# Kernel optimization log

Measured on AMD Instinct MI355X. Metric: run time of the kernel, lower is better.

## Reference

```python
import jax, jax.numpy as jnp
import numpy as np

HIDDEN = 1024
B, LQ, LK = 8, 2048, 2048


def setup_inputs() -> dict:
    key = jax.random.key(0)
    k1, k2, k3 = jax.random.split(key, 3)
    query = jax.random.normal(k1, (B, LQ, HIDDEN), dtype=jnp.float32)
    key_t = jax.random.normal(k2, (B, LK, HIDDEN), dtype=jnp.float32)
    # multiplicative binary mask on scores (float 0/1)
    attention_mask = jax.random.randint(k3, (B, LQ, LK), 0, 2).astype(jnp.float32)
    return {"query": query, "key": key_t, "attention_mask": attention_mask}


def reference(query, key, attention_mask):
    sqrt_dim = np.sqrt(HIDDEN).astype(np.float32)
    # [B, Lq, Lk] scores, scaled then multiplicatively masked (NOT additive)
    score = jnp.einsum("bqd,bkd->bqk", query, key) / sqrt_dim
    score = score * attention_mask
    attn = jax.nn.softmax(score, axis=-1)
    # NOTE: original module multiplies attn by KEY (not value)
    context = jnp.einsum("bqk,bkd->bqd", attn, key)
    return (context, attn)
```

## Files before the change

kernel.cpp:

```cpp
#include <hip/hip_runtime.h>
#include <hip/hip_bf16.h>


typedef __attribute__((ext_vector_type(8))) short bf16x8;
typedef __attribute__((ext_vector_type(4))) float f32x4;
typedef __attribute__((ext_vector_type(4))) unsigned u32x4;
typedef __attribute__((ext_vector_type(2))) unsigned u32x2;

constexpr int BATCH = 8;
constexpr int LQ    = 2048;
constexpr int LKK   = 2048;
constexpr int DH    = 1024;
constexpr float SCALE = 0.03125f;

#define GAS(p) ((const __attribute__((address_space(1))) void*)(p))
#define LAS(p) ((__attribute__((address_space(3))) void*)(p))

__device__ __forceinline__ unsigned lds_addr(const unsigned short* p) {
    return (unsigned)(unsigned long long)
        (const __attribute__((address_space(3))) unsigned short*)p;
}

__device__ __forceinline__ bf16x8 dsr_b128(unsigned off) {
    bf16x8 r;
    asm volatile("ds_read_b128 %0, %1" : "=v"(r) : "v"(off));
    return r;
}

__device__ __forceinline__ unsigned pack_bf16x2(float x0, float x1) {
    unsigned a = __builtin_bit_cast(unsigned, x0) + 0x8000u;
    unsigned b = __builtin_bit_cast(unsigned, x1) + 0x8000u;
    return __builtin_amdgcn_perm(b, a, 0x07060302u);
}

__global__ __launch_bounds__(256)
void cvt_kernel(const float* __restrict__ Q, const float* __restrict__ K,
                unsigned short* __restrict__ Qb, unsigned short* __restrict__ Kb) {
    const int bid = blockIdx.x;
    const float* src; unsigned short* dst; size_t off;
    if (bid < 4096) { src = Q; dst = Qb; off = (size_t)bid * 4096; }
    else            { src = K; dst = Kb; off = (size_t)(bid - 4096) * 4096; }
    off += (size_t)threadIdx.x * 16;
    const f32x4 a = *(const f32x4*)(src + off);
    const f32x4 b = *(const f32x4*)(src + off + 4);
    const f32x4 c = *(const f32x4*)(src + off + 8);
    const f32x4 d = *(const f32x4*)(src + off + 12);
    u32x4 v0, v1;
    v0[0] = pack_bf16x2(a[0], a[1]); v0[1] = pack_bf16x2(a[2], a[3]);
    v0[2] = pack_bf16x2(b[0], b[1]); v0[3] = pack_bf16x2(b[2], b[3]);
    v1[0] = pack_bf16x2(c[0], c[1]); v1[1] = pack_bf16x2(c[2], c[3]);
    v1[2] = pack_bf16x2(d[0], d[1]); v1[3] = pack_bf16x2(d[2], d[3]);
    *(u32x4*)(dst + off)     = v0;
    *(u32x4*)(dst + off + 8) = v1;
}

__global__ __launch_bounds__(256)
void kt_kernel(const float* __restrict__ K, unsigned short* __restrict__ KT) {
    __shared__ unsigned short T[64 * 68];
    const int b  = blockIdx.z;
    const int k0 = blockIdx.y * 64;
    const int d0 = blockIdx.x * 64;
    const int t  = threadIdx.x;
    const int k4 = (t >> 4) * 4;
    const int d4 = (t & 15) * 4;
    f32x4 rk[4];
    const float* Kp = K + ((size_t)b * LKK + k0 + k4) * DH + d0 + d4;
#pragma unroll
    for (int j = 0; j < 4; ++j) rk[j] = *(const f32x4*)(Kp + (size_t)j * DH);
#pragma unroll
    for (int c = 0; c < 4; ++c) {
        u32x2 w;
        w[0] = pack_bf16x2(rk[0][c], rk[1][c]);
        w[1] = pack_bf16x2(rk[2][c], rk[3][c]);
        *(u32x2*)&T[(d4 + c) * 68 + k4] = w;
    }
    __syncthreads();
    const int d  = t >> 2;
    const int kc = (t & 3) * 16;
    u32x2 a0 = *(const u32x2*)&T[d * 68 + kc];
    u32x2 a1 = *(const u32x2*)&T[d * 68 + kc + 4];
    u32x2 a2 = *(const u32x2*)&T[d * 68 + kc + 8];
    u32x2 a3 = *(const u32x2*)&T[d * 68 + kc + 12];
    unsigned short* dst = KT + ((size_t)b * DH + d0 + d) * LKK + k0 + kc;
    u32x4 w0; w0[0] = a0[0]; w0[1] = a0[1]; w0[2] = a1[0]; w0[3] = a1[1];
    u32x4 w1; w1[0] = a2[0]; w1[1] = a2[1]; w1[2] = a3[0]; w1[3] = a3[1];
    *(u32x4*)dst       = w0;
    *(u32x4*)(dst + 8) = w1;
}

template<int LDA, int LDB, int NT>
__device__ __forceinline__ void gemm8_mainloop(
    const unsigned short* __restrict__ Ab,
    const unsigned short* __restrict__ Bb,
    unsigned short* lA, unsigned short* lB,
    f32x4 (&acc)[8][4])
{
    const int tid  = threadIdx.x;
    const int lane = tid & 63;
    const int wid  = tid >> 6;
    const int wm   = (wid & 1) * 128;
    const int wn   = (wid >> 1) * 64;
    const int lrow = lane & 15;
    const int quad = lane >> 4;
    const int slotsw = (quad ^ ((lrow >> 1) & 3)) * 8;

    const int srow0 = wid * 32 + (lane >> 2);
    const int srow1 = srow0 + 16;
    const int sc    = ((lane & 3) ^ ((lane >> 3) & 3)) * 8;

    auto stage = [&](int I) {
        if (I >= 4 * NT) return;
        const int tile = I >> 2;
        const int h    = I & 3;
        const int kh   = h >> 1;
        const int kb   = tile * 64 + kh * 32 + sc;
        const unsigned short* s = (h & 1) ? Bb : Ab;
        const int ld            = (h & 1) ? LDB : LDA;
        unsigned short* d = ((h & 1) ? lB : lA)
                          + (tile & 1) * 16384 + kh * 8192 + wid * 1024;
        __builtin_amdgcn_global_load_lds(GAS(s + (size_t)srow0 * ld + kb), LAS(d),       16, 0, 0);
        __builtin_amdgcn_global_load_lds(GAS(s + (size_t)srow1 * ld + kb), LAS(d + 512), 16, 0, 0);
    };

#pragma unroll
    for (int i = 0; i < 8; ++i)
#pragma unroll
        for (int j = 0; j < 4; ++j) acc[i][j] = (f32x4){0.f, 0.f, 0.f, 0.f};

#pragma unroll
    for (int I = 0; I < 6; ++I) stage(I);
    asm volatile("s_waitcnt vmcnt(8)" ::: "memory");
    __builtin_amdgcn_s_barrier();

    auto tilebody = [&](int T, int par) {
        bf16x8 bfr[4];
#pragma unroll
        for (int q = 0; q < 4; ++q) {
            const int kh = (q >> 1) * 8192;
            const int mh = (q & 1) * 4;
            if ((q & 1) == 0) {
#pragma unroll
                for (int nf = 0; nf < 4; ++nf)
                    bfr[nf] = dsr_b128(lds_addr(&lB[par + kh + (wn + nf * 16 + lrow) * 32 + slotsw]));
            }
            bf16x8 af[4];
#pragma unroll
            for (int mf = 0; mf < 4; ++mf)
                af[mf] = dsr_b128(lds_addr(&lA[par + kh + (wm + (mh + mf) * 16 + lrow) * 32 + slotsw]));

            if (q == 0)      stage(4 * T + 6);
            else if (q == 1) stage(4 * T + 7);
            else if (q == 2) { stage(4 * T + 8); stage(4 * T + 9); }

            __builtin_amdgcn_s_barrier();
            asm volatile("s_waitcnt lgkmcnt(0)" ::: "memory");
            __builtin_amdgcn_sched_barrier(0);
            __builtin_amdgcn_s_setprio(1);
#pragma unroll
            for (int mf = 0; mf < 4; ++mf)
#pragma unroll
                for (int nf = 0; nf < 4; ++nf)
                    acc[mh + mf][nf] = __builtin_amdgcn_mfma_f32_16x16x32_bf16(
                        af[mf], bfr[nf], acc[mh + mf][nf], 0, 0, 0);
            __builtin_amdgcn_s_setprio(0);
            if (q == 1) {
                if (T < NT - 1)      asm volatile("s_waitcnt vmcnt(8)" ::: "memory");
                else                 asm volatile("s_waitcnt vmcnt(0)" ::: "memory");
            } else if (q == 3) {
                if (T < NT - 2)      asm volatile("s_waitcnt vmcnt(8)" ::: "memory");
                else if (T == NT - 2) asm volatile("s_waitcnt vmcnt(4)" ::: "memory");
            }
            __builtin_amdgcn_s_barrier();
        }
    };

    for (int T = 0; T < NT; T += 2) {
        tilebody(T,     0);
        tilebody(T + 1, 16384);
    }
}

__global__ __launch_bounds__(512, 2)
void qk8(const unsigned short* __restrict__ Qb, const unsigned short* __restrict__ Kb,
         const float* __restrict__ M, float* __restrict__ S) {
    __shared__ __align__(16) unsigned short lA[32768];
    __shared__ __align__(16) unsigned short lB[32768];

    const int l   = blockIdx.x;
    const int swz = (l & 7) * 64 + (l >> 3);
    const int b   = swz >> 6;
    const int my  = (swz >> 3) & 7;
    const int nx  = swz & 7;
    const int q0  = my * 256;
    const int n0  = nx * 256;

    const unsigned short* Ap = Qb + ((size_t)b * LQ  + q0) * DH;
    const unsigned short* Bp = Kb + ((size_t)b * LKK + n0) * DH;

    f32x4 acc[8][4];
    gemm8_mainloop<DH, DH, DH / 64>(Ap, Bp, lA, lB, acc);

    const int lane = threadIdx.x & 63;
    const int wid  = threadIdx.x >> 6;
    const int wm   = (wid & 1) * 128;
    const int wn   = (wid >> 1) * 64;
    const int lrow = lane & 15;
    const int quad = lane >> 4;

    const size_t base = (size_t)b * LQ * LKK;
#pragma unroll
    for (int mf = 0; mf < 8; ++mf) {
#pragma unroll
        for (int r = 0; r < 4; ++r) {
            const int row = q0 + wm + mf * 16 + quad * 4 + r;
            const size_t rb = base + (size_t)row * LKK;
#pragma unroll
            for (int nf = 0; nf < 4; ++nf) {
                const int col = n0 + wn + nf * 16 + lrow;
                S[rb + col] = acc[mf][nf][r] * SCALE * M[rb + col];
            }
        }
    }
}

__global__ __launch_bounds__(256)
void softmax_kernel(float* __restrict__ A, unsigned short* __restrict__ ab) {
    const int row  = blockIdx.x * 4 + (threadIdx.x >> 6);
    const int lane = threadIdx.x & 63;
    float* p = A + (size_t)row * LKK;

    f32x4 v[8];
#pragma unroll
    for (int i = 0; i < 8; ++i) v[i] = *(const f32x4*)(p + i * 256 + lane * 4);

    float m = v[0][0];
#pragma unroll
    for (int i = 0; i < 8; ++i)
#pragma unroll
        for (int j = 0; j < 4; ++j) m = fmaxf(m, v[i][j]);
#pragma unroll
    for (int o = 32; o >= 1; o >>= 1) m = fmaxf(m, __shfl_xor(m, o, 64));

    float s = 0.f;
#pragma unroll
    for (int i = 0; i < 8; ++i)
#pragma unroll
        for (int j = 0; j < 4; ++j) { v[i][j] = __expf(v[i][j] - m); s += v[i][j]; }
#pragma unroll
    for (int o = 32; o >= 1; o >>= 1) s += __shfl_xor(s, o, 64);
    const float inv = 1.f / s;

#pragma unroll
    for (int i = 0; i < 8; ++i) {
#pragma unroll
        for (int j = 0; j < 4; ++j) v[i][j] *= inv;
        *(f32x4*)(p + i * 256 + lane * 4) = v[i];
    }

    if (ab) {
        unsigned short* q = ab + (size_t)row * LKK;
#pragma unroll
        for (int i = 0; i < 8; ++i) {
            u32x2 w;
            w[0] = pack_bf16x2(v[i][0], v[i][1]);
            w[1] = pack_bf16x2(v[i][2], v[i][3]);
            *(u32x2*)(q + i * 256 + lane * 4) = w;
        }
    }
}

__global__ __launch_bounds__(512, 2)
void pk8(const unsigned short* __restrict__ Pb, const unsigned short* __restrict__ KT,
         float* __restrict__ C) {
    __shared__ __align__(16) unsigned short lA[32768];
    __shared__ __align__(16) unsigned short lB[32768];

    const int l   = blockIdx.x;
    const int swz = (l & 7) * 32 + (l >> 3);
    const int b   = swz >> 5;
    const int my  = (swz >> 2) & 7;
    const int nx  = swz & 3;
    const int q0  = my * 256;
    const int n0  = nx * 256;

    const unsigned short* Ap = Pb + ((size_t)b * LQ + q0) * LKK;
    const unsigned short* Bp = KT + ((size_t)b * DH + n0) * LKK;

    f32x4 acc[8][4];
    gemm8_mainloop<LKK, LKK, LKK / 64>(Ap, Bp, lA, lB, acc);

    const int lane = threadIdx.x & 63;
    const int wid  = threadIdx.x >> 6;
    const int wm   = (wid & 1) * 128;
    const int wn   = (wid >> 1) * 64;
    const int lrow = lane & 15;
    const int quad = lane >> 4;

    const size_t cb = (size_t)b * LQ * DH;
#pragma unroll
    for (int mf = 0; mf < 8; ++mf) {
#pragma unroll
        for (int r = 0; r < 4; ++r) {
            const int row = q0 + wm + mf * 16 + quad * 4 + r;
            const size_t rbase = cb + (size_t)row * DH;
#pragma unroll
            for (int nf = 0; nf < 4; ++nf)
                C[rbase + n0 + wn + nf * 16 + lrow] = acc[mf][nf][r];
        }
    }
}

constexpr int BM = 128, BN = 128, TK = 32;
constexpr int LDSS = 40;
__global__ __launch_bounds__(256, 2)
void pk_kernel(const float* __restrict__ P, const float* __restrict__ K,
               float* __restrict__ C) {
    __shared__ unsigned short lA[BM * LDSS];
    __shared__ unsigned short lB[BN * LDSS];

    const int b  = blockIdx.z;
    const int q0 = blockIdx.y * BM;
    const int n0 = blockIdx.x * BN;
    const float* Pp = P + (size_t)b * LQ * LKK + (size_t)q0 * LKK;
    const float* Kb = K + (size_t)b * LKK * DH;

    const int tid  = threadIdx.x;
    const int lane = tid & 63;
    const int wid  = tid >> 6;
    const int wm   = (wid & 1) * 64;
    const int wn   = (wid >> 1) * 64;
    const int lrow = lane & 15;
    const int quad = lane >> 4;

    f32x4 acc[4][4];
#pragma unroll
    for (int i = 0; i < 4; ++i)
#pragma unroll
        for (int j = 0; j < 4; ++j) acc[i][j] = (f32x4){0.f, 0.f, 0.f, 0.f};

    const int srow = tid >> 3;
    const int skq  = (tid & 7) << 2;
    const int tdb  = tid >> 3;
    const int tkb  = tid & 7;

    for (int k0 = 0; k0 < LKK; k0 += TK) {
        __syncthreads();
#pragma unroll
        for (int i = 0; i < 4; ++i) {
            const int row = i * 32 + srow;
            const f32x4 va = *(const f32x4*)(Pp + (size_t)row * LKK + k0 + skq);
            unsigned* pa = (unsigned*)&lA[row * LDSS + skq];
            pa[0] = pack_bf16x2(va[0], va[1]);
            pa[1] = pack_bf16x2(va[2], va[3]);
        }
        f32x4 rk[4];
#pragma unroll
        for (int j = 0; j < 4; ++j)
            rk[j] = *(const f32x4*)(Kb + (size_t)(k0 + tkb * 4 + j) * DH + n0 + tdb * 4);
#pragma unroll
        for (int c = 0; c < 4; ++c) {
            unsigned* pb = (unsigned*)&lB[(tdb * 4 + c) * LDSS + tkb * 4];
            pb[0] = pack_bf16x2(rk[0][c], rk[1][c]);
            pb[1] = pack_bf16x2(rk[2][c], rk[3][c]);
        }
        __syncthreads();

        bf16x8 af[4], bfr[4];
#pragma unroll
        for (int i = 0; i < 4; ++i) {
            af[i]  = *(const bf16x8*)&lA[(wm + i * 16 + lrow) * LDSS + quad * 8];
            bfr[i] = *(const bf16x8*)&lB[(wn + i * 16 + lrow) * LDSS + quad * 8];
        }
#pragma unroll
        for (int i = 0; i < 4; ++i)
#pragma unroll
            for (int j = 0; j < 4; ++j)
                acc[i][j] = __builtin_amdgcn_mfma_f32_16x16x32_bf16(af[i], bfr[j], acc[i][j], 0, 0, 0);
    }

    const size_t cb = (size_t)b * LQ * DH;
#pragma unroll
    for (int i = 0; i < 4; ++i) {
#pragma unroll
        for (int r = 0; r < 4; ++r) {
            const int row = q0 + wm + i * 16 + quad * 4 + r;
            const size_t rbase = cb + (size_t)row * DH;
#pragma unroll
            for (int j = 0; j < 4; ++j)
                C[rbase + n0 + wn + j * 16 + lrow] = acc[i][j][r];
        }
    }
}

extern "C" void kernel_launch(void* const* d_in, const int* in_sizes, int n_in,
                              void* d_out, int out_size, void* d_ws, size_t ws_size,
                              hipStream_t stream) {
    const float* Q = (const float*)d_in[0];
    const float* K = (const float*)d_in[1];
    const float* M = (const float*)d_in[2];

    constexpr size_t QEL  = (size_t)BATCH * LQ * DH;
    constexpr size_t AEL  = (size_t)BATCH * LQ * LKK;
    constexpr size_t KTEL = (size_t)BATCH * DH * LKK;

    float* ctx  = (float*)d_out;
    float* attn = ctx + QEL;

    unsigned short* Qb = (unsigned short*)ctx;
    unsigned short* Kb = Qb + QEL;

    const bool wsOK = ws_size >= (KTEL + AEL) * sizeof(unsigned short);
    unsigned short* KT = (unsigned short*)d_ws;
    unsigned short* ab = KT + KTEL;

    cvt_kernel<<<dim3(8192), 256, 0, stream>>>(Q, K, Qb, Kb);
    if (wsOK)
        kt_kernel<<<dim3(DH / 64, LKK / 64, BATCH), 256, 0, stream>>>(K, KT);
    qk8<<<dim3(BATCH * (LQ / 256) * (LKK / 256)), 512, 0, stream>>>(Qb, Kb, M, attn);
    softmax_kernel<<<dim3(BATCH * LQ / 4), 256, 0, stream>>>(attn, wsOK ? ab : nullptr);
    if (wsOK)
        pk8<<<dim3(BATCH * (LQ / 256) * (DH / 256)), 512, 0, stream>>>(ab, KT, ctx);
    else
        pk_kernel<<<dim3(DH / BN, LQ / BM, BATCH), 256, 0, stream>>>(attn, K, ctx);
}
```

Before: 574.7 us.

## Fuse exp into QK epilogue, defer softmax normalization into PV epilogue

The QK GEMM epilogue now applies scale, mask and exp directly and writes bf16 unnormalized probabilities, replacing the fp32 score buffer and the separate max/exp softmax pass. A lighter sum_norm kernel reads the bf16 values, computes the per-row reciprocal sum, writes the normalized fp32 attention output and stores the reciprocals. The PV GEMM multiplies its output rows by those reciprocals. K's bf16 conversion also moves into the transpose kernel, so K is read once instead of twice. The aim is to cut large fp32 round trips through HBM. The cost is dropping max subtraction, which risks overflow for larger score ranges, and deriving the attention output from bf16-rounded exponentials, which lowers its precision.

```diff
diff --git a/kernel.cpp b/kernel.cpp
--- a/kernel.cpp
+++ b/kernel.cpp
@@ -31,6 +31,10 @@
     unsigned a = __builtin_bit_cast(unsigned, x0) + 0x8000u;
     unsigned b = __builtin_bit_cast(unsigned, x1) + 0x8000u;
     return __builtin_amdgcn_perm(b, a, 0x07060302u);
+}
+
+__device__ __forceinline__ unsigned short pack_bf16(float x) {
+    return (unsigned short)((__builtin_bit_cast(unsigned, x) + 0x8000u) >> 16);
 }
 
 __global__ __launch_bounds__(256)
@@ -55,7 +59,8 @@
 }
 
 __global__ __launch_bounds__(256)
-void kt_kernel(const float* __restrict__ K, unsigned short* __restrict__ KT) {
+void kt_kernel(const float* __restrict__ K, unsigned short* __restrict__ KT,
+               unsigned short* __restrict__ Kb) {
     __shared__ unsigned short T[64 * 68];
     const int b  = blockIdx.z;
     const int k0 = blockIdx.y * 64;
@@ -67,6 +72,14 @@
     const float* Kp = K + ((size_t)b * LKK + k0 + k4) * DH + d0 + d4;
 #pragma unroll
     for (int j = 0; j < 4; ++j) rk[j] = *(const f32x4*)(Kp + (size_t)j * DH);
+    unsigned short* Kbp = Kb + ((size_t)b * LKK + k0 + k4) * DH + d0 + d4;
+#pragma unroll
+    for (int j = 0; j < 4; ++j) {
+        u32x2 w;
+        w[0] = pack_bf16x2(rk[j][0], rk[j][1]);
+        w[1] = pack_bf16x2(rk[j][2], rk[j][3]);
+        *(u32x2*)(Kbp + (size_t)j * DH) = w;
+    }
 #pragma unroll
     for (int c = 0; c < 4; ++c) {
         u32x2 w;
@@ -164,10 +177,10 @@
                         af[mf], bfr[nf], acc[mh + mf][nf], 0, 0, 0);
             __builtin_amdgcn_s_setprio(0);
             if (q == 1) {
-                if (T < NT - 1)      asm volatile("s_waitcnt vmcnt(8)" ::: "memory");
-                else                 asm volatile("s_waitcnt vmcnt(0)" ::: "memory");
+                if (T < NT - 1)       asm volatile("s_waitcnt vmcnt(8)" ::: "memory");
+                else                  asm volatile("s_waitcnt vmcnt(0)" ::: "memory");
             } else if (q == 3) {
-                if (T < NT - 2)      asm volatile("s_waitcnt vmcnt(8)" ::: "memory");
+                if (T < NT - 2)       asm volatile("s_waitcnt vmcnt(8)" ::: "memory");
                 else if (T == NT - 2) asm volatile("s_waitcnt vmcnt(4)" ::: "memory");
             }
             __builtin_amdgcn_s_barrier();
@@ -180,9 +193,11 @@
     }
 }
 
+template<bool FUSED>
 __global__ __launch_bounds__(512, 2)
 void qk8(const unsigned short* __restrict__ Qb, const unsigned short* __restrict__ Kb,
-         const float* __restrict__ M, float* __restrict__ S) {
+         const float* __restrict__ M, float* __restrict__ S,
+         unsigned short* __restrict__ ab) {
     __shared__ __align__(16) unsigned short lA[32768];
     __shared__ __align__(16) unsigned short lB[32768];
 
@@ -217,10 +232,55 @@
 #pragma unroll
             for (int nf = 0; nf < 4; ++nf) {
                 const int col = n0 + wn + nf * 16 + lrow;
-                S[rb + col] = acc[mf][nf][r] * SCALE * M[rb + col];
+                if (FUSED) {
+                    const float e = __expf(acc[mf][nf][r] * SCALE * M[rb + col]);
+                    ab[rb + col] = pack_bf16(e);
+                } else {
+                    S[rb + col] = acc[mf][nf][r] * SCALE * M[rb + col];
+                }
             }
         }
     }
+}
+
+__global__ __launch_bounds__(256)
+void sum_norm(const unsigned short* __restrict__ ab, float* __restrict__ attn,
+              float* __restrict__ inv) {
+    const int row  = blockIdx.x * 4 + (threadIdx.x >> 6);
+    const int lane = threadIdx.x & 63;
+    const unsigned short* q = ab + (size_t)row * LKK;
+
+    u32x4 w[4];
+#pragma unroll
+    for (int i = 0; i < 4; ++i) w[i] = *(const u32x4*)(q + i * 512 + lane * 8);
+
+    float v[32];
+    float s = 0.f;
+#pragma unroll
+    for (int i = 0; i < 4; ++i)
+#pragma unroll
+        for (int j = 0; j < 4; ++j) {
+            const unsigned u = w[i][j];
+            const float lo = __builtin_bit_cast(float, u << 16);
+            const float hi = __builtin_bit_cast(float, u & 0xFFFF0000u);
+            v[i * 8 + j * 2]     = lo;
+            v[i * 8 + j * 2 + 1] = hi;
+            s += lo + hi;
+        }
+#pragma unroll
+    for (int o = 32; o >= 1; o >>= 1) s += __shfl_xor(s, o, 64);
+    const float iv = 1.f / s;
+
+    float* p = attn + (size_t)row * LKK;
+#pragma unroll
+    for (int i = 0; i < 4; ++i) {
+        f32x4 o0, o1;
+#pragma unroll
+        for (int j = 0; j < 4; ++j) { o0[j] = v[i * 8 + j] * iv; o1[j] = v[i * 8 + 4 + j] * iv; }
+        *(f32x4*)(p + i * 512 + lane * 8)     = o0;
+        *(f32x4*)(p + i * 512 + lane * 8 + 4) = o1;
+    }
+    if (lane == 0) inv[row] = iv;
 }
 
 __global__ __launch_bounds__(256)
@@ -271,7 +331,7 @@
 
 __global__ __launch_bounds__(512, 2)
 void pk8(const unsigned short* __restrict__ Pb, const unsigned short* __restrict__ KT,
-         float* __restrict__ C) {
+         const float* __restrict__ Inv, float* __restrict__ C) {
     __shared__ __align__(16) unsigned short lA[32768];
     __shared__ __align__(16) unsigned short lB[32768];
 
@@ -296,16 +356,18 @@
     const int lrow = lane & 15;
     const int quad = lane >> 4;
 
+    const float* Ivp = Inv + (size_t)b * LQ;
     const size_t cb = (size_t)b * LQ * DH;
 #pragma unroll
     for (int mf = 0; mf < 8; ++mf) {
 #pragma unroll
         for (int r = 0; r < 4; ++r) {
             const int row = q0 + wm + mf * 16 + quad * 4 + r;
+            const float iv = Ivp[row];
             const size_t rbase = cb + (size_t)row * DH;
 #pragma unroll
             for (int nf = 0; nf < 4; ++nf)
-                C[rbase + n0 + wn + nf * 16 + lrow] = acc[mf][nf][r];
+                C[rbase + n0 + wn + nf * 16 + lrow] = acc[mf][nf][r] * iv;
         }
     }
 }
@@ -402,6 +464,7 @@
     constexpr size_t QEL  = (size_t)BATCH * LQ * DH;
     constexpr size_t AEL  = (size_t)BATCH * LQ * LKK;
     constexpr size_t KTEL = (size_t)BATCH * DH * LKK;
+    constexpr size_t REL  = (size_t)BATCH * LQ;
 
     float* ctx  = (float*)d_out;
     float* attn = ctx + QEL;
@@ -409,17 +472,24 @@
     unsigned short* Qb = (unsigned short*)ctx;
     unsigned short* Kb = Qb + QEL;
 
-    const bool wsOK = ws_size >= (KTEL + AEL) * sizeof(unsigned short);
+    const bool wsOK = ws_size >= (KTEL + AEL) * sizeof(unsigned short)
+                               + REL * sizeof(float);
     unsigned short* KT = (unsigned short*)d_ws;
     unsigned short* ab = KT + KTEL;
-
-    cvt_kernel<<<dim3(8192), 256, 0, stream>>>(Q, K, Qb, Kb);
-    if (wsOK)
-        kt_kernel<<<dim3(DH / 64, LKK / 64, BATCH), 256, 0, stream>>>(K, KT);
-    qk8<<<dim3(BATCH * (LQ / 256) * (LKK / 256)), 512, 0, stream>>>(Qb, Kb, M, attn);
-    softmax_kernel<<<dim3(BATCH * LQ / 4), 256, 0, stream>>>(attn, wsOK ? ab : nullptr);
-    if (wsOK)
-        pk8<<<dim3(BATCH * (LQ / 256) * (DH / 256)), 512, 0, stream>>>(ab, KT, ctx);
-    else
+    float* inv = (float*)(ab + AEL);
+
+    if (wsOK) {
+        cvt_kernel<<<dim3(4096), 256, 0, stream>>>(Q, K, Qb, Kb);
+        kt_kernel<<<dim3(DH / 64, LKK / 64, BATCH), 256, 0, stream>>>(K, KT, Kb);
+        qk8<true><<<dim3(BATCH * (LQ / 256) * (LKK / 256)), 512, 0, stream>>>(
+            Qb, Kb, M, nullptr, ab);
+        sum_norm<<<dim3(BATCH * LQ / 4), 256, 0, stream>>>(ab, attn, inv);
+        pk8<<<dim3(BATCH * (LQ / 256) * (DH / 256)), 512, 0, stream>>>(ab, KT, inv, ctx);
+    } else {
+        cvt_kernel<<<dim3(8192), 256, 0, stream>>>(Q, K, Qb, Kb);
+        qk8<false><<<dim3(BATCH * (LQ / 256) * (LKK / 256)), 512, 0, stream>>>(
+            Qb, Kb, M, attn, nullptr);
+        softmax_kernel<<<dim3(BATCH * LQ / 4), 256, 0, stream>>>(attn, nullptr);
         pk_kernel<<<dim3(DH / BN, LQ / BM, BATCH), 256, 0, stream>>>(attn, K, ctx);
-}
+    }
+}
```

Measured after the change: 540.0 us. 6.0% less time.
